# Optimization experiments

Hardware: AMD Instinct MI355X
Metric: run time of the kernel (lower is better)

## Reference

```python
import jax, jax.numpy as jnp
import numpy as np

STRIDES = (8, 16, 32)
NUM_CLASSES = 80
BINS = 16
TOPK = 10
W_CLS, W_IOU, W_DFL = 0.5, 7.5, 1.5
EPS = 1e-9


def make_grid(H, W, stride):
    ys, xs = jnp.meshgrid(jnp.arange(H, dtype=jnp.float32),
                          jnp.arange(W, dtype=jnp.float32), indexing='ij')
    return jnp.stack([(xs + 0.5) * stride, (ys + 0.5) * stride], -1).reshape(-1, 2)


def decode_dfl(dfl, grid, stride):
    # dfl: (B, 64, H, W), channel layout coord-major (4 coords x 16 bins)
    B, C, H, W = dfl.shape
    prob = jax.nn.softmax(dfl.reshape(B, 4, BINS, H, W), axis=2)
    proj = jnp.arange(BINS, dtype=dfl.dtype)
    dist = jnp.einsum('bkchw,c->bkhw', prob, proj)              # expected bin value
    dist = dist.transpose(0, 2, 3, 1).reshape(B, H * W, 4) * stride  # (B,N,4) ltrb px
    cx, cy = grid[:, 0], grid[:, 1]
    return jnp.stack([cx - dist[..., 0], cy - dist[..., 1],
                      cx + dist[..., 2], cy + dist[..., 3]], -1)   # (B,N,4) xyxy


def pairwise_iou(gt, pr, eps=1e-7):
    # gt (B,G,4), pr (B,N,4) -> (B,G,N)
    lt = jnp.maximum(gt[:, :, None, :2], pr[:, None, :, :2])
    rb = jnp.minimum(gt[:, :, None, 2:], pr[:, None, :, 2:])
    wh = jnp.clip(rb - lt, 0.0)
    inter = wh[..., 0] * wh[..., 1]
    ag = jnp.clip(gt[..., 2] - gt[..., 0], 0) * jnp.clip(gt[..., 3] - gt[..., 1], 0)
    ap = jnp.clip(pr[..., 2] - pr[..., 0], 0) * jnp.clip(pr[..., 3] - pr[..., 1], 0)
    return inter / (ag[:, :, None] + ap[:, None, :] - inter + eps)


def ciou(b1, b2, eps=1e-7):
    # elementwise CIoU over (...,4) xyxy boxes
    w1, h1 = b1[..., 2] - b1[..., 0], b1[..., 3] - b1[..., 1]
    w2, h2 = b2[..., 2] - b2[..., 0], b2[..., 3] - b2[..., 1]
    lt = jnp.maximum(b1[..., :2], b2[..., :2])
    rb = jnp.minimum(b1[..., 2:], b2[..., 2:])
    wh = jnp.clip(rb - lt, 0.0)
    inter = wh[..., 0] * wh[..., 1]
    union = w1 * h1 + w2 * h2 - inter + eps
    iou = inter / union
    cw = jnp.maximum(b1[..., 2], b2[..., 2]) - jnp.minimum(b1[..., 0], b2[..., 0])
    ch = jnp.maximum(b1[..., 3], b2[..., 3]) - jnp.minimum(b1[..., 1], b2[..., 1])
    c2 = cw * cw + ch * ch + eps
    rho2 = ((b1[..., 0] + b1[..., 2] - b2[..., 0] - b2[..., 2]) ** 2 +
            (b1[..., 1] + b1[..., 3] - b2[..., 1] - b2[..., 3]) ** 2) / 4.0
    v = (4.0 / np.pi ** 2) * (jnp.arctan(w2 / (h2 + eps)) - jnp.arctan(w1 / (h1 + eps))) ** 2
    a = jax.lax.stop_gradient(v / (v - iou + (1.0 + eps)))
    return iou - rho2 / c2 - a * v


def tal_assign(scores, pred_boxes, gt_bboxes, gt_labels, grid, topk=TOPK, alpha=0.5, beta=6.0):
    B, N, C = scores.shape
    G = gt_bboxes.shape[1]
    mask_gt = gt_bboxes.sum(-1) > 0                                    # (B,G) zero-padded gts
    cx, cy = grid[None, None, :, 0], grid[None, None, :, 1]
    in_gts = ((cx > gt_bboxes[..., 0:1]) & (cx < gt_bboxes[..., 2:3]) &
              (cy > gt_bboxes[..., 1:2]) & (cy < gt_bboxes[..., 3:4]))  # (B,G,N)
    iou = pairwise_iou(gt_bboxes, pred_boxes)                          # (B,G,N)
    probs = jax.nn.sigmoid(scores)                                     # (B,N,C)
    idx = jnp.broadcast_to(gt_labels[:, None, :], (B, N, G))
    cls_g = jnp.take_along_axis(probs, idx, axis=2).transpose(0, 2, 1)  # (B,G,N)
    valid = in_gts & mask_gt[:, :, None]
    align = jnp.where(valid, (cls_g ** alpha) * (iou ** beta), 0.0)
    vals, idxk = jax.lax.top_k(align, topk)                            # (B,G,K)
    bi = jnp.arange(B)[:, None, None]
    gi = jnp.arange(G)[None, :, None]
    topk_mask = jnp.zeros((B, G, N), bool).at[bi, gi, idxk].set(vals > EPS)
    mask_pos = topk_mask & valid
    # resolve anchors assigned to multiple gts: keep gt with highest IoU
    multi = mask_pos.sum(1) > 1                                        # (B,N)
    best_gt = jnp.argmax(iou, axis=1)                                  # (B,N)
    best_oh = best_gt[:, None, :] == jnp.arange(G)[None, :, None]      # (B,G,N)
    mask_pos = jnp.where(multi[:, None, :], best_oh, mask_pos)
    fg_mask = mask_pos.any(1)                                          # (B,N)
    matched = jnp.argmax(mask_pos, axis=1)                             # (B,N)
    matched_gt_inds = jnp.where(fg_mask, matched, -1)
    target_bboxes = jnp.take_along_axis(gt_bboxes, matched[:, :, None], axis=1)
    target_labels = jnp.take_along_axis(gt_labels, matched, axis=1)
    t1h = jax.nn.one_hot(target_labels, C, dtype=scores.dtype) * fg_mask[..., None]
    align_pos = align * mask_pos
    pos_align_max = align_pos.max(2, keepdims=True)                    # per-gt max metric
    pos_iou_max = (iou * mask_pos).max(2, keepdims=True)               # per-gt max overlap
    norm = (align_pos * pos_iou_max / (pos_align_max + EPS)).max(1)    # (B,N)
    target_scores = t1h * norm[..., None]
    return target_scores, target_bboxes, fg_mask, matched_gt_inds


def yolo_loss(p0, p1, p2, gt_bboxes, gt_labels):
    scores_l, dfl_l, boxes_l, grids_l = [], [], [], []
    for p, s in zip((p0, p1, p2), STRIDES):
        B, _, H, W = p.shape
        N = H * W
        dfl, cls = p[:, :64], p[:, 64:64 + NUM_CLASSES]
        grid = make_grid(H, W, s)
        boxes_l.append(decode_dfl(dfl, grid, s))
        scores_l.append(cls.transpose(0, 2, 3, 1).reshape(B, N, NUM_CLASSES))
        dfl_l.append(dfl.transpose(0, 2, 3, 1).reshape(B, N, 4, BINS))
        grids_l.append(grid)
    all_scores = jnp.concatenate(scores_l, 1)      # (B,Nt,80)
    all_dfl = jnp.concatenate(dfl_l, 1)            # (B,Nt,4,16)
    pred_boxes = jnp.concatenate(boxes_l, 1)       # (B,Nt,4)
    grid = jnp.concatenate(grids_l, 0)             # (Nt,2)
    t_scores, t_boxes, fg, matched = tal_assign(all_scores, pred_boxes, gt_bboxes, gt_labels, grid)
    fgf = fg.astype(all_scores.dtype)
    num_pos = jnp.maximum(fgf.sum(), 1.0)
    # BCE with logits, stable form, soft targets
    s = all_scores
    bce = jnp.clip(s, 0.0) - s * t_scores + jnp.log1p(jnp.exp(-jnp.abs(s)))
    loss_cls = bce.sum() / num_pos
    loss_iou = ((1.0 - ciou(pred_boxes, t_boxes)) * fgf).sum() / num_pos  # mean over positives
    # DFL soft targets (original calls _make_dfl_targets with stride=1)
    m = jnp.clip(matched, 0)
    boxes = jnp.take_along_axis(gt_bboxes, m[:, :, None], axis=1)         # (B,Nt,4)
    gcx, gcy = grid[None, :, 0], grid[None, :, 1]
    dists = jnp.stack([jnp.clip(gcx - boxes[..., 0], 0.0),
                       jnp.clip(gcy - boxes[..., 1], 0.0),
                       jnp.clip(boxes[..., 2] - gcx, 0.0),
                       jnp.clip(boxes[..., 3] - gcy, 0.0)], -1)           # (B,Nt,4)
    tb = jnp.clip(dists, 0.0, BINS - 1 - 1e-6)
    lo = jnp.floor(tb)
    a = tb - lo
    li = lo.astype(jnp.int32)
    ui = jnp.minimum(li + 1, BINS - 1)
    td = (jax.nn.one_hot(li, BINS, dtype=tb.dtype) * (1.0 - a)[..., None] +
          jax.nn.one_hot(ui, BINS, dtype=tb.dtype) * a[..., None])        # (B,Nt,4,16)
    td = td * fgf[:, :, None, None]
    lsm = jax.nn.log_softmax(all_dfl, axis=-1)
    loss_dfl = -(td * lsm).sum() / num_pos
    return jnp.stack([W_IOU * loss_iou, W_CLS * loss_cls, W_DFL * loss_dfl])


def setup_inputs() -> dict:
    key = jax.random.key(0)
    k = jax.random.split(key, 6)
    B, G = 32, 32
    p0 = jax.random.normal(k[0], (B, 144, 80, 80), jnp.float32)
    p1 = jax.random.normal(k[1], (B, 144, 40, 40), jnp.float32)
    p2 = jax.random.normal(k[2], (B, 144, 20, 20), jnp.float32)
    c = jax.random.uniform(k[3], (B, G, 2), minval=60.0, maxval=580.0)
    wh = jax.random.uniform(k[4], (B, G, 2), minval=20.0, maxval=200.0)
    gt_bboxes = jnp.concatenate([jnp.clip(c - wh / 2, 0.0, 640.0),
                                 jnp.clip(c + wh / 2, 0.0, 640.0)], -1)
    gt_labels = jax.random.randint(k[5], (B, G), 0, NUM_CLASSES)
    return {'p0': p0, 'p1': p1, 'p2': p2, 'gt_bboxes': gt_bboxes, 'gt_labels': gt_labels}


def reference(p0, p1, p2, gt_bboxes, gt_labels):
    return yolo_loss(p0, p1, p2, gt_bboxes, gt_labels)
```

## Files before the change

kernel.cpp:

```cpp
#include <hip/hip_runtime.h>
#include <hip/hip_bf16.h>

#define NB 32
#define NG 32
#define NC 80
#define NTOT 8400
#define CH 144
#define BN (NB * NTOT)

#define TILES_PER_B 34
#define NBLK1 (NB * TILES_PER_B)
#define NBLKN 33
#define NBLK3 (NBLKN * NB)

struct AInfo {
    const float* base;
    int hw;
    int off;
    float cx, cy, stride;
};

__device__ __forceinline__ AInfo anchor_info(int n, int b, const float* p0, const float* p1, const float* p2) {
    AInfo ai;
    if (n < 6400) {
        int x = n % 80, y = n / 80;
        ai.hw = 6400; ai.off = n;
        ai.cx = (x + 0.5f) * 8.0f; ai.cy = (y + 0.5f) * 8.0f; ai.stride = 8.0f;
        ai.base = p0 + (size_t)b * CH * 6400;
    } else if (n < 8000) {
        int m = n - 6400; int x = m % 40, y = m / 40;
        ai.hw = 1600; ai.off = m;
        ai.cx = (x + 0.5f) * 16.0f; ai.cy = (y + 0.5f) * 16.0f; ai.stride = 16.0f;
        ai.base = p1 + (size_t)b * CH * 1600;
    } else {
        int m = n - 8000; int x = m % 20, y = m / 20;
        ai.hw = 400; ai.off = m;
        ai.cx = (x + 0.5f) * 32.0f; ai.cy = (y + 0.5f) * 32.0f; ai.stride = 32.0f;
        ai.base = p2 + (size_t)b * CH * 400;
    }
    return ai;
}

__device__ __forceinline__ void ins10(float a[10], float v) {
    if (v > a[9]) {
        a[9] = v;
#pragma unroll
        for (int i = 8; i >= 0; i--) {
            if (a[i + 1] > a[i]) { float t = a[i]; a[i] = a[i + 1]; a[i + 1] = t; }
        }
    }
}

__device__ __forceinline__ float iou_fn(float4 gb, float4 pb, float ap) {
    float ag = fmaxf(gb.z - gb.x, 0.f) * fmaxf(gb.w - gb.y, 0.f);
    float iw = fmaxf(fminf(gb.z, pb.z) - fmaxf(gb.x, pb.x), 0.f);
    float ih = fmaxf(fminf(gb.w, pb.w) - fmaxf(gb.y, pb.y), 0.f);
    float inter = iw * ih;
    return inter / (ag + ap - inter + 1e-7f);
}

__device__ __forceinline__ float align_metric(float s, float iou) {
    float sg = 1.f / (1.f + __expf(-s));
    float i2 = iou * iou;
    return sqrtf(sg) * i2 * i2 * i2;
}

__device__ __forceinline__ float ciou_fn(float4 p, float4 t) {
    float w1 = p.z - p.x, h1 = p.w - p.y;
    float w2 = t.z - t.x, h2 = t.w - t.y;
    float iw = fmaxf(fminf(p.z, t.z) - fmaxf(p.x, t.x), 0.f);
    float ih = fmaxf(fminf(p.w, t.w) - fmaxf(p.y, t.y), 0.f);
    float inter = iw * ih;
    float un = w1 * h1 + w2 * h2 - inter + 1e-7f;
    float iou = inter / un;
    float cw = fmaxf(p.z, t.z) - fminf(p.x, t.x);
    float chh = fmaxf(p.w, t.w) - fminf(p.y, t.y);
    float c2 = cw * cw + chh * chh + 1e-7f;
    float dx = p.x + p.z - t.x - t.z, dy = p.y + p.w - t.y - t.w;
    float rho2 = (dx * dx + dy * dy) * 0.25f;
    float da = atanf(w2 / (h2 + 1e-7f)) - atanf(w1 / (h1 + 1e-7f));
    float v = 0.4052847345693511f * da * da;
    float al = v / (v - iou + 1.f + 1e-7f);
    return iou - rho2 / c2 - al * v;
}

__device__ __forceinline__ float softplus4(float4 v) {
    float r = 0.f, s;
    s = v.x; r += fmaxf(s, 0.f) + __logf(1.f + __expf(-fabsf(s)));
    s = v.y; r += fmaxf(s, 0.f) + __logf(1.f + __expf(-fabsf(s)));
    s = v.z; r += fmaxf(s, 0.f) + __logf(1.f + __expf(-fabsf(s)));
    s = v.w; r += fmaxf(s, 0.f) + __logf(1.f + __expf(-fabsf(s)));
    return r;
}

__global__ __launch_bounds__(256) void k1_fused(
    const float* __restrict__ p0, const float* __restrict__ p1, const float* __restrict__ p2,
    float* __restrict__ pred, float* __restrict__ lse, float* __restrict__ part_bce,
    float* __restrict__ posA, float* __restrict__ posI) {
    int blk = blockIdx.x;
    if (blk == 0) {
        for (int i = threadIdx.x; i < NB * NG; i += 256) { posA[i] = 0.f; posI[i] = 0.f; }
    }
    int b = blk / TILES_PER_B;
    int tile = blk - b * TILES_PER_B;
    const float* base; int hw, o0, lvl_off, W; float spx;
    if (tile < 25)      { base = p0; hw = 6400; o0 = tile * 256;        lvl_off = 0;    W = 80; spx = 8.f;  }
    else if (tile < 32) { base = p1; hw = 1600; o0 = (tile - 25) * 256; lvl_off = 6400; W = 40; spx = 16.f; }
    else                { base = p2; hw = 400;  o0 = (tile - 32) * 256; lvl_off = 8000; W = 20; spx = 32.f; }
    base += (size_t)b * CH * hw;
    int valid = min(256, hw - o0);
    int valid4 = valid >> 2;
    int hw4 = hw >> 2, o04 = o0 >> 2;
    const float4* base4 = (const float4*)base;

    int g4 = threadIdx.x >> 2, k = threadIdx.x & 3;
    if (g4 < valid4) {
        float4 v[16];
#pragma unroll
        for (int j = 0; j < 16; j++)
            v[j] = base4[(size_t)(k * 16 + j) * hw4 + o04 + g4];
        float dist[4], lv[4];
#pragma unroll
        for (int c = 0; c < 4; c++) {
            float mx = -1e30f;
#pragma unroll
            for (int j = 0; j < 16; j++) { float x = ((const float*)&v[j])[c]; mx = fmaxf(mx, x); }
            float se = 0.f, we = 0.f;
#pragma unroll
            for (int j = 0; j < 16; j++) {
                float e = __expf(((const float*)&v[j])[c] - mx);
                se += e; we += e * (float)j;
            }
            dist[c] = we / se * spx;
            lv[c] = mx + __logf(se);
        }
#pragma unroll
        for (int c = 0; c < 4; c++) {
            int nl = o0 + g4 * 4 + c;
            int x = nl % W, y = nl / W;
            float cx = (x + 0.5f) * spx, cy = (y + 0.5f) * spx;
            float ctr = (k & 1) ? cy : cx;
            size_t ai = (size_t)b * NTOT + lvl_off + nl;
            pred[ai * 4 + k] = (k < 2) ? (ctr - dist[c]) : (ctr + dist[c]);
            lse[ai * 4 + k] = lv[c];
        }
    }

    int wv = threadIdx.x >> 6, f4 = threadIdx.x & 63;
    float bce = 0.f;
    if (f4 < valid4) {
        const float4* clsb = base4 + (size_t)64 * hw4 + o04 + f4;
        float4 vv[10];
#pragma unroll
        for (int i = 0; i < 10; i++) vv[i] = clsb[(size_t)(wv + i * 4) * hw4];
#pragma unroll
        for (int i = 0; i < 10; i++) bce += softplus4(vv[i]);
#pragma unroll
        for (int i = 0; i < 10; i++) vv[i] = clsb[(size_t)(wv + (i + 10) * 4) * hw4];
#pragma unroll
        for (int i = 0; i < 10; i++) bce += softplus4(vv[i]);
    }
#pragma unroll
    for (int off = 32; off > 0; off >>= 1) bce += __shfl_xor(bce, off, 64);
    __shared__ float red[4];
    if ((threadIdx.x & 63) == 0) red[threadIdx.x >> 6] = bce;
    __syncthreads();
    if (threadIdx.x == 0)
        part_bce[blk] = red[0] + red[1] + red[2] + red[3];
}

__global__ __launch_bounds__(256) void k2_thr(
    const float* __restrict__ p0, const float* __restrict__ p1, const float* __restrict__ p2,
    const float* __restrict__ gtb, const int* __restrict__ gtl,
    const float* __restrict__ pred, float* __restrict__ thr) {
    int g = blockIdx.x, b = blockIdx.y;
    const float* gb = gtb + (size_t)(b * NG + g) * 4;
    float gx1 = gb[0], gy1 = gb[1], gx2 = gb[2], gy2 = gb[3];
    bool vg = (gx1 + gy1 + gx2 + gy2) > 0.f;
    int label = gtl[b * NG + g];
    float4 gb4 = { gx1, gy1, gx2, gy2 };
    const float* bases[3] = { p0 + (size_t)b * CH * 6400,
                              p1 + (size_t)b * CH * 1600,
                              p2 + (size_t)b * CH * 400 };
    const int Ws[3] = { 80, 40, 20 }, hws[3] = { 6400, 1600, 400 }, loff[3] = { 0, 6400, 8000 };
    const float ss[3] = { 8.f, 16.f, 32.f };
    int X0[3], W_[3], Y0[3], CNT[3];
    int tot = 0;
#pragma unroll
    for (int l = 0; l < 3; l++) {
        int x0 = 0, x1 = -1, y0 = 0, y1 = -1;
        if (vg) {
            float s = ss[l];
            x0 = max(0, (int)floorf(gx1 / s - 0.5f));
            x1 = min(Ws[l] - 1, (int)floorf(gx2 / s - 0.5f) + 1);
            y0 = max(0, (int)floorf(gy1 / s - 0.5f));
            y1 = min(Ws[l] - 1, (int)floorf(gy2 / s - 0.5f) + 1);
        }
        int w = x1 - x0 + 1, h = y1 - y0 + 1;
        X0[l] = x0; Y0[l] = y0; W_[l] = w;
        CNT[l] = (w > 0 && h > 0) ? w * h : 0;
        tot += CNT[l];
    }
    float top[10];
#pragma unroll
    for (int i = 0; i < 10; i++) top[i] = 0.f;
    const float4* pred4 = (const float4*)pred + (size_t)b * NTOT;
    for (int i = threadIdx.x; i < tot; i += 256) {
        int l = 0, r = i;
        if (r >= CNT[0]) { r -= CNT[0]; l = 1; if (r >= CNT[1]) { r -= CNT[1]; l = 2; } }
        int w = W_[l];
        int y = Y0[l] + r / w, x = X0[l] + r % w;
        float s = ss[l];
        float cx = (x + 0.5f) * s, cy = (y + 0.5f) * s;
        int nr = y * Ws[l] + x;
        float4 pb = pred4[loff[l] + nr];
        float sc = bases[l][(size_t)(64 + label) * hws[l] + nr];
        float ap = fmaxf(pb.z - pb.x, 0.f) * fmaxf(pb.w - pb.y, 0.f);
        float iou = iou_fn(gb4, pb, ap);
        bool ing = (cx > gx1) && (cx < gx2) && (cy > gy1) && (cy < gy2);
        float al = 0.f;
        if (ing && vg) al = align_metric(sc, iou);
        ins10(top, al);
    }
    __shared__ float s_top[256 * 10];
#pragma unroll
    for (int i = 0; i < 10; i++) s_top[threadIdx.x * 10 + i] = top[i];
    __syncthreads();
    if (threadIdx.x < 64) {
        float mt[10];
#pragma unroll
        for (int i = 0; i < 10; i++) mt[i] = 0.f;
        for (int src = threadIdx.x; src < 256; src += 64)
#pragma unroll
            for (int i = 0; i < 10; i++) ins10(mt, s_top[src * 10 + i]);
        float thrv = 0.f;
        for (int r = 0; r < 10; r++) {
            unsigned long long key = ((unsigned long long)__float_as_uint(mt[0]) << 32) | (unsigned)threadIdx.x;
#pragma unroll
            for (int off = 32; off > 0; off >>= 1) {
                unsigned long long o = __shfl_xor(key, off, 64);
                if (o > key) key = o;
            }
            thrv = __uint_as_float((unsigned)(key >> 32));
            if ((key & 63ULL) == (unsigned long long)threadIdx.x) {
#pragma unroll
                for (int i = 0; i < 9; i++) mt[i] = mt[i + 1];
                mt[9] = 0.f;
            }
        }
        if (threadIdx.x == 0) thr[b * NG + g] = thrv;
    }
}

__global__ __launch_bounds__(256) void k3_mask(
    const float* __restrict__ p0, const float* __restrict__ p1, const float* __restrict__ p2,
    const float* __restrict__ thr, const float* __restrict__ pred,
    const float* __restrict__ gtb, const int* __restrict__ gtl,
    unsigned* __restrict__ maskv, int* __restrict__ matchedv,
    float* __restrict__ posA, float* __restrict__ posI, unsigned* __restrict__ partN) {
    int b = blockIdx.y;
    int n = blockIdx.x * 256 + threadIdx.x;
    __shared__ float s_thr[NG];
    __shared__ float4 s_gt[NG];
    __shared__ int s_lab[NG];
    if (threadIdx.x < NG) {
        s_thr[threadIdx.x] = thr[b * NG + threadIdx.x];
        float4 gb4 = ((const float4*)gtb)[b * NG + threadIdx.x];
        if (!((gb4.x + gb4.y + gb4.z + gb4.w) > 0.f))
            gb4 = make_float4(1e30f, 1e30f, -1e30f, -1e30f);
        s_gt[threadIdx.x] = gb4;
        s_lab[threadIdx.x] = gtl[b * NG + threadIdx.x];
    }
    __syncthreads();
    bool fg = false;
    if (n < NTOT) {
        AInfo ai = anchor_info(n, b, p0, p1, p2);
        float4 pb = ((const float4*)pred)[(size_t)b * NTOT + n];
        float ap = fmaxf(pb.z - pb.x, 0.f) * fmaxf(pb.w - pb.y, 0.f);
        unsigned m = 0;
        for (int g = 0; g < NG; g++) {
            float4 gb4 = s_gt[g];
            bool ing = (ai.cx > gb4.x) && (ai.cx < gb4.z) && (ai.cy > gb4.y) && (ai.cy < gb4.w);
            if (__any(ing)) {
                float al = 0.f;
                if (ing) {
                    float iou = iou_fn(gb4, pb, ap);
                    float s = ai.base[(size_t)(64 + s_lab[g]) * ai.hw + ai.off];
                    al = align_metric(s, iou);
                }
                if (al >= s_thr[g] && al > 1e-9f) m |= (1u << g);
            }
        }
        int cnt = __popc(m);
        int matched = -1;
        if (cnt > 0) {
            if (cnt > 1) {
                float best = -1.f; int bg = 0;
                for (int g = 0; g < NG; g++) {
                    float iou = iou_fn(s_gt[g], pb, ap);
                    if (iou > best) { best = iou; bg = g; }
                }
                m = 1u << bg;
            }
            for (int g = 0; g < NG; g++) {
                if ((m >> g) & 1u) {
                    float4 gb4 = s_gt[g];
                    float iou = iou_fn(gb4, pb, ap);
                    bool ing = (ai.cx > gb4.x) && (ai.cx < gb4.z) && (ai.cy > gb4.y) && (ai.cy < gb4.w);
                    float al = 0.f;
                    if (ing) {
                        float s = ai.base[(size_t)(64 + s_lab[g]) * ai.hw + ai.off];
                        al = align_metric(s, iou);
                    }
                    atomicMax((int*)&posI[b * NG + g], __float_as_int(iou));
                    atomicMax((int*)&posA[b * NG + g], __float_as_int(al));
                }
            }
            matched = __ffs(m) - 1;
            fg = true;
        }
        maskv[(size_t)b * NTOT + n] = m;
        matchedv[(size_t)b * NTOT + n] = matched;
    }
    unsigned long long bal = __ballot(fg);
    __shared__ unsigned redN[4];
    if ((threadIdx.x & 63) == 0) redN[threadIdx.x >> 6] = (unsigned)__popcll(bal);
    __syncthreads();
    if (threadIdx.x == 0)
        partN[blockIdx.y * gridDim.x + blockIdx.x] = redN[0] + redN[1] + redN[2] + redN[3];
}

__global__ __launch_bounds__(256) void k5_loss(
    const float* __restrict__ p0, const float* __restrict__ p1, const float* __restrict__ p2,
    const unsigned* __restrict__ maskv, const int* __restrict__ matchedv,
    const float* __restrict__ posA, const float* __restrict__ posI,
    const float* __restrict__ gtb, const int* __restrict__ gtl,
    const float* __restrict__ pred, const float* __restrict__ lse,
    float* __restrict__ part_corr, float* __restrict__ part_liou, float* __restrict__ part_ldfl) {
    int b = blockIdx.y;
    int n = blockIdx.x * 256 + threadIdx.x;
    __shared__ float4 s_gt[NG];
    __shared__ int s_lab[NG];
    __shared__ float s_pa[NG], s_pi[NG];
    if (threadIdx.x < NG) {
        s_gt[threadIdx.x] = ((const float4*)gtb)[b * NG + threadIdx.x];
        s_lab[threadIdx.x] = gtl[b * NG + threadIdx.x];
        s_pa[threadIdx.x] = posA[b * NG + threadIdx.x];
        s_pi[threadIdx.x] = posI[b * NG + threadIdx.x];
    }
    __syncthreads();
    float corr = 0.f, liou = 0.f, ldfl = 0.f;
    if (n < NTOT) {
        int mt = matchedv[(size_t)b * NTOT + n];
        if (mt >= 0) {
            AInfo ai = anchor_info(n, b, p0, p1, p2);
            const float* base = ai.base + ai.off;
            float4 pb = ((const float4*)pred)[(size_t)b * NTOT + n];
            float ap = fmaxf(pb.z - pb.x, 0.f) * fmaxf(pb.w - pb.y, 0.f);
            unsigned m = maskv[(size_t)b * NTOT + n];
            float nrm = 0.f;
            unsigned mm = m;
            while (mm) {
                int g = __ffs(mm) - 1; mm &= mm - 1;
                float4 gb4 = s_gt[g];
                float iou = iou_fn(gb4, pb, ap);
                bool ing = (ai.cx > gb4.x) && (ai.cx < gb4.z) && (ai.cy > gb4.y) && (ai.cy < gb4.w);
                float al = 0.f;
                if (ing) {
                    float s = base[(size_t)(64 + s_lab[g]) * ai.hw];
                    al = align_metric(s, iou);
                }
                nrm = fmaxf(nrm, al * s_pi[g] / (s_pa[g] + 1e-9f));
            }
            float s = base[(size_t)(64 + s_lab[mt]) * ai.hw];
            corr = s * nrm;
            float4 tb = s_gt[mt];
            liou = 1.f - ciou_fn(pb, tb);
            float4 l4 = ((const float4*)lse)[(size_t)b * NTOT + n];
            float lv[4] = { l4.x, l4.y, l4.z, l4.w };
            float d[4] = { fmaxf(ai.cx - tb.x, 0.f), fmaxf(ai.cy - tb.y, 0.f),
                           fmaxf(tb.z - ai.cx, 0.f), fmaxf(tb.w - ai.cy, 0.f) };
            float Ls[8];
            int li4[4], ui4[4]; float afr4[4];
#pragma unroll
            for (int k = 0; k < 4; k++) {
                float tbk = fminf(d[k], 14.999999f);
                float lo = floorf(tbk);
                afr4[k] = tbk - lo;
                li4[k] = (int)lo;
                ui4[k] = min(li4[k] + 1, 15);
            }
#pragma unroll
            for (int k = 0; k < 4; k++) {
                Ls[k * 2]     = base[(size_t)(k * 16 + li4[k]) * ai.hw];
                Ls[k * 2 + 1] = base[(size_t)(k * 16 + ui4[k]) * ai.hw];
            }
#pragma unroll
            for (int k = 0; k < 4; k++)
                ldfl += lv[k] - ((1.f - afr4[k]) * Ls[k * 2] + afr4[k] * Ls[k * 2 + 1]);
        }
    }
#pragma unroll
    for (int off = 32; off > 0; off >>= 1) {
        corr += __shfl_xor(corr, off, 64);
        liou += __shfl_xor(liou, off, 64);
        ldfl += __shfl_xor(ldfl, off, 64);
    }
    __shared__ float rc[4], ri[4], rd[4];
    if ((threadIdx.x & 63) == 0) {
        int w = threadIdx.x >> 6;
        rc[w] = corr; ri[w] = liou; rd[w] = ldfl;
    }
    __syncthreads();
    if (threadIdx.x == 0) {
        int blk = blockIdx.y * gridDim.x + blockIdx.x;
        part_corr[blk] = rc[0] + rc[1] + rc[2] + rc[3];
        part_liou[blk] = ri[0] + ri[1] + ri[2] + ri[3];
        part_ldfl[blk] = rd[0] + rd[1] + rd[2] + rd[3];
    }
}

__global__ __launch_bounds__(256) void k6_final(
    const float* __restrict__ part_bce, const float* __restrict__ part_corr,
    const float* __restrict__ part_liou, const float* __restrict__ part_ldfl,
    const unsigned* __restrict__ partN, float* __restrict__ out) {
    double bce = 0.0, corr = 0.0, liou = 0.0, ldfl = 0.0, np = 0.0;
    for (int i = threadIdx.x; i < NBLK1; i += 256) bce += (double)part_bce[i];
    for (int i = threadIdx.x; i < NBLK3; i += 256) {
        corr += (double)part_corr[i];
        liou += (double)part_liou[i];
        ldfl += (double)part_ldfl[i];
        np   += (double)partN[i];
    }
#pragma unroll
    for (int off = 32; off > 0; off >>= 1) {
        bce  += __shfl_xor(bce, off, 64);
        corr += __shfl_xor(corr, off, 64);
        liou += __shfl_xor(liou, off, 64);
        ldfl += __shfl_xor(ldfl, off, 64);
        np   += __shfl_xor(np, off, 64);
    }
    __shared__ double rb[4], rc[4], ri[4], rd[4], rn[4];
    if ((threadIdx.x & 63) == 0) {
        int w = threadIdx.x >> 6;
        rb[w] = bce; rc[w] = corr; ri[w] = liou; rd[w] = ldfl; rn[w] = np;
    }
    __syncthreads();
    if (threadIdx.x == 0) {
        bce  = rb[0] + rb[1] + rb[2] + rb[3];
        corr = rc[0] + rc[1] + rc[2] + rc[3];
        liou = ri[0] + ri[1] + ri[2] + ri[3];
        ldfl = rd[0] + rd[1] + rd[2] + rd[3];
        np   = rn[0] + rn[1] + rn[2] + rn[3];
        if (np < 1.0) np = 1.0;
        out[0] = (float)(7.5 * liou / np);
        out[1] = (float)(0.5 * (bce - corr) / np);
        out[2] = (float)(1.5 * ldfl / np);
    }
}

extern "C" void kernel_launch(void* const* d_in, const int* in_sizes, int n_in,
                              void* d_out, int out_size, void* d_ws, size_t ws_size,
                              hipStream_t stream) {
    const float* p0 = (const float*)d_in[0];
    const float* p1 = (const float*)d_in[1];
    const float* p2 = (const float*)d_in[2];
    const float* gtb = (const float*)d_in[3];
    const int* gtl = (const int*)d_in[4];
    float* out = (float*)d_out;

    char* w = (char*)d_ws;
    float* pred = (float*)w;
    float* lse = pred + (size_t)BN * 4;
    float* thr = lse + (size_t)BN * 4;
    float* posA = thr + NB * NG;
    float* posI = posA + NB * NG;
    unsigned* maskv = (unsigned*)(posI + NB * NG);
    int* matchedv = (int*)(maskv + BN);
    float* part_bce = (float*)(matchedv + BN);
    float* part_corr = part_bce + NBLK1;
    float* part_liou = part_corr + NBLK3;
    float* part_ldfl = part_liou + NBLK3;
    unsigned* partN = (unsigned*)(part_ldfl + NBLK3);

    hipLaunchKernelGGL(k1_fused, dim3(NBLK1), dim3(256), 0, stream,
                       p0, p1, p2, pred, lse, part_bce, posA, posI);
    hipLaunchKernelGGL(k2_thr, dim3(NG, NB), dim3(256), 0, stream,
                       p0, p1, p2, gtb, gtl, pred, thr);
    hipLaunchKernelGGL(k3_mask, dim3(NBLKN, NB), dim3(256), 0, stream,
                       p0, p1, p2, thr, pred, gtb, gtl, maskv, matchedv, posA, posI, partN);
    hipLaunchKernelGGL(k5_loss, dim3(NBLKN, NB), dim3(256), 0, stream,
                       p0, p1, p2, maskv, matchedv, posA, posI, gtb, gtl, pred, lse,
                       part_corr, part_liou, part_ldfl);
    hipLaunchKernelGGL(k6_final, dim3(1), dim3(256), 0, stream,
                       part_bce, part_corr, part_liou, part_ldfl, partN, out);
}
```

Baseline: 253.9 us.

## Split fused DFL/BCE kernel into separate DFL and flat grid-stride BCE kernels

Splits the first kernel into a DFL-decode kernel and a separate class-BCE kernel. The BCE kernel walks all class logits as a flat float4 index space over all levels and batches, so every thread has uniform work with 8 loads in flight, instead of per-tile waves that sit idle on partial tiles. The DFL kernel also remaps threads so each wave handles one coordinate over consecutive anchors, which makes the pred/lse stores follow a different pattern, and it uses launch_bounds(256,1). The cost is one more kernel launch and the class logits no longer sharing a block with the DFL reads.

```diff
diff --git a/kernel.cpp b/kernel.cpp
--- a/kernel.cpp
+++ b/kernel.cpp
@@ -9,7 +9,8 @@
 #define BN (NB * NTOT)
 
 #define TILES_PER_B 34
-#define NBLK1 (NB * TILES_PER_B)
+#define NBLK1A (NB * TILES_PER_B)
+#define NBLK1B 2625
 #define NBLKN 33
 #define NBLK3 (NBLKN * NB)
 
@@ -93,9 +94,9 @@
     return r;
 }
 
-__global__ __launch_bounds__(256) void k1_fused(
+__global__ __launch_bounds__(256, 1) void k1a_dfl(
     const float* __restrict__ p0, const float* __restrict__ p1, const float* __restrict__ p2,
-    float* __restrict__ pred, float* __restrict__ lse, float* __restrict__ part_bce,
+    float* __restrict__ pred, float* __restrict__ lse,
     float* __restrict__ posA, float* __restrict__ posI) {
     int blk = blockIdx.x;
     if (blk == 0) {
@@ -113,7 +114,8 @@
     int hw4 = hw >> 2, o04 = o0 >> 2;
     const float4* base4 = (const float4*)base;
 
-    int g4 = threadIdx.x >> 2, k = threadIdx.x & 3;
+    int k = threadIdx.x >> 6;
+    int g4 = threadIdx.x & 63;
     if (g4 < valid4) {
         float4 v[16];
 #pragma unroll
@@ -145,28 +147,36 @@
             lse[ai * 4 + k] = lv[c];
         }
     }
-
-    int wv = threadIdx.x >> 6, f4 = threadIdx.x & 63;
+}
+
+__global__ __launch_bounds__(256) void k1b_bce(
+    const float* __restrict__ p0, const float* __restrict__ p1, const float* __restrict__ p2,
+    float* __restrict__ part_bce) {
+    const int T = NBLK1B * 256;
+    int tid = blockIdx.x * 256 + threadIdx.x;
+    const int E0 = 4096000, E1 = 1024000;
+    float4 vv[8];
+#pragma unroll
+    for (int q = 0; q < 8; q++) {
+        int i = tid + q * T;
+        const float4* p; int slab4, bstride4, coff4, li;
+        if (i < E0)            { p = (const float4*)p0; slab4 = 128000; bstride4 = 230400; coff4 = 102400; li = i; }
+        else if (i < E0 + E1)  { p = (const float4*)p1; slab4 = 32000;  bstride4 = 57600;  coff4 = 25600;  li = i - E0; }
+        else                   { p = (const float4*)p2; slab4 = 8000;   bstride4 = 14400;  coff4 = 6400;   li = i - E0 - E1; }
+        int b = li / slab4;
+        int r = li - b * slab4;
+        vv[q] = p[(size_t)b * bstride4 + coff4 + r];
+    }
     float bce = 0.f;
-    if (f4 < valid4) {
-        const float4* clsb = base4 + (size_t)64 * hw4 + o04 + f4;
-        float4 vv[10];
-#pragma unroll
-        for (int i = 0; i < 10; i++) vv[i] = clsb[(size_t)(wv + i * 4) * hw4];
-#pragma unroll
-        for (int i = 0; i < 10; i++) bce += softplus4(vv[i]);
-#pragma unroll
-        for (int i = 0; i < 10; i++) vv[i] = clsb[(size_t)(wv + (i + 10) * 4) * hw4];
-#pragma unroll
-        for (int i = 0; i < 10; i++) bce += softplus4(vv[i]);
-    }
+#pragma unroll
+    for (int q = 0; q < 8; q++) bce += softplus4(vv[q]);
 #pragma unroll
     for (int off = 32; off > 0; off >>= 1) bce += __shfl_xor(bce, off, 64);
     __shared__ float red[4];
     if ((threadIdx.x & 63) == 0) red[threadIdx.x >> 6] = bce;
     __syncthreads();
     if (threadIdx.x == 0)
-        part_bce[blk] = red[0] + red[1] + red[2] + red[3];
+        part_bce[blockIdx.x] = red[0] + red[1] + red[2] + red[3];
 }
 
 __global__ __launch_bounds__(256) void k2_thr(
@@ -425,7 +435,7 @@
     const float* __restrict__ part_liou, const float* __restrict__ part_ldfl,
     const unsigned* __restrict__ partN, float* __restrict__ out) {
     double bce = 0.0, corr = 0.0, liou = 0.0, ldfl = 0.0, np = 0.0;
-    for (int i = threadIdx.x; i < NBLK1; i += 256) bce += (double)part_bce[i];
+    for (int i = threadIdx.x; i < NBLK1B; i += 256) bce += (double)part_bce[i];
     for (int i = threadIdx.x; i < NBLK3; i += 256) {
         corr += (double)part_corr[i];
         liou += (double)part_liou[i];
@@ -478,13 +488,15 @@
     unsigned* maskv = (unsigned*)(posI + NB * NG);
     int* matchedv = (int*)(maskv + BN);
     float* part_bce = (float*)(matchedv + BN);
-    float* part_corr = part_bce + NBLK1;
+    float* part_corr = part_bce + NBLK1B;
     float* part_liou = part_corr + NBLK3;
     float* part_ldfl = part_liou + NBLK3;
     unsigned* partN = (unsigned*)(part_ldfl + NBLK3);
 
-    hipLaunchKernelGGL(k1_fused, dim3(NBLK1), dim3(256), 0, stream,
-                       p0, p1, p2, pred, lse, part_bce, posA, posI);
+    hipLaunchKernelGGL(k1a_dfl, dim3(NBLK1A), dim3(256), 0, stream,
+                       p0, p1, p2, pred, lse, posA, posI);
+    hipLaunchKernelGGL(k1b_bce, dim3(NBLK1B), dim3(256), 0, stream,
+                       p0, p1, p2, part_bce);
     hipLaunchKernelGGL(k2_thr, dim3(NG, NB), dim3(256), 0, stream,
                        p0, p1, p2, gtb, gtl, pred, thr);
     hipLaunchKernelGGL(k3_mask, dim3(NBLKN, NB), dim3(256), 0, stream,
```

New measurement: 258.1 us. About the same (+1.7%).
